# Kernel tuning notes

Hardware: AMD Instinct MI355X
Metric: run time of the kernel (lower is better)

Reference implementation:

```python
import jax, jax.numpy as jnp
import numpy as np

D_MODEL = 1024
N_REG = 8
D_REG = 32
LN_EPS = 1e-5


def setup_inputs() -> dict:
    key = jax.random.key(0)
    ks = jax.random.split(key, 14)
    s = 0.02
    return {
        "x": jax.random.normal(ks[0], (8, 2048, D_MODEL), dtype=jnp.float32),
        "ln_w": jnp.ones((D_MODEL,), jnp.float32),
        "ln_b": jnp.zeros((D_MODEL,), jnp.float32),
        "Wrq": jax.random.normal(ks[1], (N_REG, D_MODEL), jnp.float32) * s,
        "brq": jax.random.normal(ks[2], (N_REG,), jnp.float32) * s,
        "Wrp": jax.random.normal(ks[3], (D_MODEL, D_REG), jnp.float32) * s,
        "brp": jax.random.normal(ks[4], (D_MODEL,), jnp.float32) * s,
        "Wwq": jax.random.normal(ks[5], (N_REG, D_MODEL), jnp.float32) * s,
        "bwq": jax.random.normal(ks[6], (N_REG,), jnp.float32) * s,
        "Wwv": jax.random.normal(ks[7], (D_REG, D_MODEL), jnp.float32) * s,
        "bwv": jax.random.normal(ks[8], (D_REG,), jnp.float32) * s,
        "Wwg": jax.random.normal(ks[9], (1, D_MODEL), jnp.float32) * s,
        "bwg": jnp.full((1,), -3.0, jnp.float32),
        "mix": jnp.asarray(0.001, jnp.float32),
    }


def _layernorm(x, w, b):
    mu = jnp.mean(x, axis=-1, keepdims=True)
    var = jnp.mean(jnp.square(x - mu), axis=-1, keepdims=True)
    return (x - mu) * jax.lax.rsqrt(var + LN_EPS) * w + b


def _forward(x, ln_w, ln_b, Wrq, brq, Wrp, brp, Wwq, bwq, Wwv, bwv, Wwg, bwg, mix):
    B, L, D = x.shape
    h = _layernorm(x, ln_w, ln_b)  # (B,L,D)
    # Precompute all per-timestep projections as big GEMMs (same math as per-step Linear)
    r_w = jax.nn.softmax(jnp.einsum("bld,rd->blr", h, Wrq) + brq, axis=-1)  # (B,L,R)
    w_w = jax.nn.softmax(jnp.einsum("bld,rd->blr", h, Wwq) + bwq, axis=-1)  # (B,L,R)
    w_v = jnp.einsum("bld,kd->blk", h, Wwv) + bwv                           # (B,L,Dr)
    w_g = jax.nn.sigmoid(jnp.einsum("bld,od->blo", h, Wwg) + bwg)           # (B,L,1)

    def step(registers, inputs):
        rw_t, ww_t, wv_t, wg_t = inputs  # (B,R), (B,R), (B,Dr), (B,1)
        r_v = jnp.einsum("br,brd->bd", rw_t, registers)  # read (B,Dr)
        us = (ww_t * wg_t)[..., None]                     # (B,R,1)
        new_regs = (1.0 - us) * registers + us * wv_t[:, None, :]
        return new_regs, r_v

    init_regs = jnp.zeros((B, N_REG, D_REG), x.dtype)
    seq = (
        jnp.moveaxis(r_w, 1, 0),
        jnp.moveaxis(w_w, 1, 0),
        jnp.moveaxis(w_v, 1, 0),
        jnp.moveaxis(w_g, 1, 0),
    )
    _, r_vs = jax.lax.scan(step, init_regs, seq)  # (L,B,Dr)
    r_vs = jnp.moveaxis(r_vs, 0, 1)               # (B,L,Dr)
    r_out = jnp.einsum("blk,dk->bld", r_vs, Wrp) + brp  # read_proj
    return mix * r_out


def reference(x, ln_w, ln_b, Wrq, brq, Wrp, brp, Wwq, bwq, Wwv, bwv, Wwg, bwg, mix):
    return _forward(x, ln_w, ln_b, Wrq, brq, Wrp, brp, Wwq, bwq, Wwv, bwv, Wwg, bwg, mix)
```

## Files before the change

kernel.cpp:

```cpp
#include <hip/hip_runtime.h>

#define D_MODEL 1024
#define L_SEQ   2048
#define N_BATCH 8
#define N_TOK   (N_BATCH * L_SEQ)
#define N_REGS  8
#define D_REG   32
#define N_CHUNK 64
#define CHUNK   32
#define LN_EPS  1e-5f

__device__ __forceinline__ float wred(float v) {
    #pragma unroll
    for (int off = 32; off > 0; off >>= 1) v += __shfl_xor(v, off, 64);
    return v;
}

__device__ __forceinline__ float sigmoidf(float z) {
    return 1.f / (1.f + expf(-z));
}

__global__ __launch_bounds__(256) void k_prep(
    const float* __restrict__ ln_w, const float* __restrict__ ln_b,
    const float* __restrict__ Wrq,  const float* __restrict__ brq,
    const float* __restrict__ Wwq,  const float* __restrict__ bwq,
    const float* __restrict__ Wwv,  const float* __restrict__ bwv,
    const float* __restrict__ Wwg,  const float* __restrict__ bwg,
    float* __restrict__ Wpp, float* __restrict__ c1, float* __restrict__ c2)
{
    const int f = blockIdx.x;
    const int g = f / 13, i = f % 13;

    const float* wrow = nullptr; float bias = 0.f;
    if (f < 8)        { wrow = Wrq + f * D_MODEL;        bias = brq[f]; }
    else if (f < 16)  { wrow = Wwq + (f - 8) * D_MODEL;  bias = bwq[f - 8]; }
    else if (f == 16) { wrow = Wwg;                      bias = bwg[0]; }
    else if (f < 49)  { wrow = Wwv + (f - 17) * D_MODEL; bias = bwv[f - 17]; }

    float p1 = 0.f, p2 = 0.f;
    #pragma unroll
    for (int j = 0; j < 4; ++j) {
        const int k = j * 256 + threadIdx.x;
        float w  = wrow ? wrow[k] : 0.f;
        float wg = w * ln_w[k];
        Wpp[((size_t)(g * D_MODEL + k)) * 16 + i] = wg;
        p1 += wg;
        p2 = fmaf(w, ln_b[k], p2);
    }
    p1 = wred(p1); p2 = wred(p2);

    __shared__ float r1[4], r2[4];
    const int l = threadIdx.x & 63, w = threadIdx.x >> 6;
    if (l == 0) { r1[w] = p1; r2[w] = p2; }
    __syncthreads();
    if (threadIdx.x == 0) {
        c1[f] = r1[0] + r1[1] + r1[2] + r1[3];
        c2[f] = r2[0] + r2[1] + r2[2] + r2[3] + bias;
    }
}

__global__ __launch_bounds__(1024) void k_lnproj2(
    const float* __restrict__ x,
    const float* __restrict__ Wpp,
    const float* __restrict__ c1, const float* __restrict__ c2,
    float* __restrict__ rw_o, float* __restrict__ us_o, float* __restrict__ wv_o)
{
    const int tid  = threadIdx.x;
    const int lane = tid & 63;
    const int wv   = tid >> 6;
    const int g    = wv & 3;
    const int kh   = wv >> 2;
    const int tok  = blockIdx.x * 64 + lane;

    const int gs  = __builtin_amdgcn_readfirstlane(g);
    const int khs = __builtin_amdgcn_readfirstlane(kh);

    const float4* xr = reinterpret_cast<const float4*>(x + (size_t)tok * D_MODEL + khs * 256);
    const float4* wr = reinterpret_cast<const float4*>(Wpp) + (size_t)(gs * D_MODEL + khs * 256) * 4;

    float acc[13];
    #pragma unroll
    for (int i = 0; i < 13; ++i) acc[i] = 0.f;
    float sum = 0.f, ss = 0.f;

    for (int kk = 0; kk < 256; kk += 16) {
        float xb[16];
        #pragma unroll
        for (int u2 = 0; u2 < 4; ++u2) {
            float4 v = xr[(kk >> 2) + u2];
            xb[u2 * 4 + 0] = v.x; xb[u2 * 4 + 1] = v.y;
            xb[u2 * 4 + 2] = v.z; xb[u2 * 4 + 3] = v.w;
        }
        #pragma unroll
        for (int u = 0; u < 16; ++u) {
            const int k = kk + u;
            float4 wa = wr[k * 4 + 0];
            float4 wb = wr[k * 4 + 1];
            float4 wc = wr[k * 4 + 2];
            float  wd = reinterpret_cast<const float*>(wr + k * 4 + 3)[0];
            const float xs = xb[u];
            acc[0]  = fmaf(xs, wa.x, acc[0]);
            acc[1]  = fmaf(xs, wa.y, acc[1]);
            acc[2]  = fmaf(xs, wa.z, acc[2]);
            acc[3]  = fmaf(xs, wa.w, acc[3]);
            acc[4]  = fmaf(xs, wb.x, acc[4]);
            acc[5]  = fmaf(xs, wb.y, acc[5]);
            acc[6]  = fmaf(xs, wb.z, acc[6]);
            acc[7]  = fmaf(xs, wb.w, acc[7]);
            acc[8]  = fmaf(xs, wc.x, acc[8]);
            acc[9]  = fmaf(xs, wc.y, acc[9]);
            acc[10] = fmaf(xs, wc.z, acc[10]);
            acc[11] = fmaf(xs, wc.w, acc[11]);
            acc[12] = fmaf(xs, wd,   acc[12]);
            sum += xs;
            ss = fmaf(xs, xs, ss);
        }
    }

    __shared__ float S[64][56];
    if (kh == 0) {
        #pragma unroll
        for (int i = 0; i < 13; ++i) S[lane][g * 13 + i] = acc[i];
        if (g == 0) { S[lane][52] = sum; S[lane][53] = ss; }
    }
    __syncthreads();
    #pragma unroll
    for (int ph = 1; ph < 4; ++ph) {
        if (kh == ph) {
            #pragma unroll
            for (int i = 0; i < 13; ++i) S[lane][g * 13 + i] += acc[i];
            if (g == 0) { S[lane][52] += sum; S[lane][53] += ss; }
        }
        __syncthreads();
    }

    if (tid < 256) {
        const int t  = tid & 63;
        const int q  = tid >> 6;
        const int tg = blockIdx.x * 64 + t;

        const float tsum = S[t][52], tss = S[t][53];
        const float mu  = tsum * (1.f / D_MODEL);
        const float var = tss * (1.f / D_MODEL) - mu * mu;
        const float rs  = rsqrtf(var + LN_EPS);

        if (q == 0) {
            float lg[8];
            #pragma unroll
            for (int r = 0; r < 8; ++r)
                lg[r] = rs * (S[t][r] - mu * c1[r]) + c2[r];
            float m = lg[0];
            #pragma unroll
            for (int r = 1; r < 8; ++r) m = fmaxf(m, lg[r]);
            float sm = 0.f;
            #pragma unroll
            for (int r = 0; r < 8; ++r) { lg[r] = expf(lg[r] - m); sm += lg[r]; }
            float inv = 1.f / sm;
            float4* o = reinterpret_cast<float4*>(rw_o + (size_t)tg * 8);
            o[0] = make_float4(lg[0]*inv, lg[1]*inv, lg[2]*inv, lg[3]*inv);
            o[1] = make_float4(lg[4]*inv, lg[5]*inv, lg[6]*inv, lg[7]*inv);
        } else if (q == 1) {
            float lg[8];
            #pragma unroll
            for (int r = 0; r < 8; ++r)
                lg[r] = rs * (S[t][8 + r] - mu * c1[8 + r]) + c2[8 + r];
            float gl = rs * (S[t][16] - mu * c1[16]) + c2[16];
            float m = lg[0];
            #pragma unroll
            for (int r = 1; r < 8; ++r) m = fmaxf(m, lg[r]);
            float sm = 0.f;
            #pragma unroll
            for (int r = 0; r < 8; ++r) { lg[r] = expf(lg[r] - m); sm += lg[r]; }
            float inv = sigmoidf(gl) / sm;
            float4* o = reinterpret_cast<float4*>(us_o + (size_t)tg * 8);
            o[0] = make_float4(lg[0]*inv, lg[1]*inv, lg[2]*inv, lg[3]*inv);
            o[1] = make_float4(lg[4]*inv, lg[5]*inv, lg[6]*inv, lg[7]*inv);
        } else {
            const int f0 = 17 + (q - 2) * 16;
            float4* o = reinterpret_cast<float4*>(wv_o + (size_t)tg * 32 + (q - 2) * 16);
            #pragma unroll
            for (int jq = 0; jq < 4; ++jq) {
                float v0 = rs * (S[t][f0 + jq*4 + 0] - mu * c1[f0 + jq*4 + 0]) + c2[f0 + jq*4 + 0];
                float v1 = rs * (S[t][f0 + jq*4 + 1] - mu * c1[f0 + jq*4 + 1]) + c2[f0 + jq*4 + 1];
                float v2 = rs * (S[t][f0 + jq*4 + 2] - mu * c1[f0 + jq*4 + 2]) + c2[f0 + jq*4 + 2];
                float v3 = rs * (S[t][f0 + jq*4 + 3] - mu * c1[f0 + jq*4 + 3]) + c2[f0 + jq*4 + 3];
                o[jq] = make_float4(v0, v1, v2, v3);
            }
        }
    }
}

__global__ __launch_bounds__(256) void k_chunk(
    const float* __restrict__ us, const float* __restrict__ wv,
    float* __restrict__ A, float* __restrict__ Bc)
{
    const int gid  = blockIdx.x * 256 + threadIdx.x;
    const int k    = gid & 31;
    const int unit = gid >> 5;
    const int ch   = unit & 63;
    const int br   = unit >> 6;
    const int b    = br >> 3, r = br & 7;
    const int t0   = ch * CHUNK;

    const float* usp = us + ((size_t)(b * L_SEQ + t0)) * 8 + r;
    const float* wvp = wv + ((size_t)(b * L_SEQ + t0)) * 32 + k;

    float Aacc = 1.f, Bacc = 0.f;
    #pragma unroll 4
    for (int t = 0; t < CHUNK; ++t) {
        float u = usp[t * 8];
        float w = wvp[t * 32];
        float a = 1.f - u;
        Aacc *= a;
        Bacc = a * Bacc + u * w;
    }
    Bc[(size_t)unit * 32 + k] = Bacc;
    if (k == 0) A[unit] = Aacc;
}

__global__ __launch_bounds__(64) void k_chain(
    const float* __restrict__ A, const float* __restrict__ Bc,
    float* __restrict__ S0)
{
    const int gid = blockIdx.x * 64 + threadIdx.x;
    const int k   = gid & 31;
    const int br  = gid >> 5;
    float st = 0.f;
    #pragma unroll 4
    for (int ch = 0; ch < N_CHUNK; ++ch) {
        const int unit = br * N_CHUNK + ch;
        S0[(size_t)unit * 32 + k] = st;
        st = A[unit] * st + Bc[(size_t)unit * 32 + k];
    }
}

__global__ __launch_bounds__(64) void k_replay(
    const float* __restrict__ rw, const float* __restrict__ us,
    const float* __restrict__ wv, const float* __restrict__ S0,
    float* __restrict__ rvs)
{
    const int gid  = blockIdx.x * 64 + threadIdx.x;
    const int k    = gid & 31;
    const int unit = gid >> 5;
    const int ch   = unit & 63;
    const int b    = unit >> 6;

    float s[8];
    #pragma unroll
    for (int r = 0; r < 8; ++r)
        s[r] = S0[((size_t)((b * 8 + r) * N_CHUNK) + ch) * 32 + k];

    const int t0 = b * L_SEQ + ch * CHUNK;
    const float* rwp = rw + (size_t)t0 * 8;
    const float* usp = us + (size_t)t0 * 8;
    const float* wvp = wv + (size_t)t0 * 32 + k;
    float*       rvp = rvs + (size_t)t0 * 32 + k;

    for (int t = 0; t < CHUNK; ++t) {
        float4 rw0 = reinterpret_cast<const float4*>(rwp + t * 8)[0];
        float4 rw1 = reinterpret_cast<const float4*>(rwp + t * 8)[1];
        float4 us0 = reinterpret_cast<const float4*>(usp + t * 8)[0];
        float4 us1 = reinterpret_cast<const float4*>(usp + t * 8)[1];
        float  w   = wvp[t * 32];

        float rv = rw0.x*s[0] + rw0.y*s[1] + rw0.z*s[2] + rw0.w*s[3]
                 + rw1.x*s[4] + rw1.y*s[5] + rw1.z*s[6] + rw1.w*s[7];
        rvp[t * 32] = rv;

        s[0] = (1.f - us0.x)*s[0] + us0.x*w;
        s[1] = (1.f - us0.y)*s[1] + us0.y*w;
        s[2] = (1.f - us0.z)*s[2] + us0.z*w;
        s[3] = (1.f - us0.w)*s[3] + us0.w*w;
        s[4] = (1.f - us1.x)*s[4] + us1.x*w;
        s[5] = (1.f - us1.y)*s[5] + us1.y*w;
        s[6] = (1.f - us1.z)*s[6] + us1.z*w;
        s[7] = (1.f - us1.w)*s[7] + us1.w*w;
    }
}

__global__ __launch_bounds__(256) void k_outproj(
    const float* __restrict__ rvs, const float* __restrict__ Wrp,
    const float* __restrict__ brp, const float* __restrict__ mix_p,
    float* __restrict__ out)
{
    const int d    = blockIdx.y * 256 + threadIdx.x;
    const int tok0 = blockIdx.x * 64;

    float4 wr[8];
    #pragma unroll
    for (int q = 0; q < 8; ++q)
        wr[q] = reinterpret_cast<const float4*>(Wrp)[(size_t)d * 8 + q];

    const float bias = brp[d];
    const float mix  = mix_p[0];

    for (int t = 0; t < 64; ++t) {
        const float4* rv = reinterpret_cast<const float4*>(rvs + (size_t)(tok0 + t) * 32);
        float acc = 0.f;
        #pragma unroll
        for (int q = 0; q < 8; ++q) {
            float4 v = rv[q];
            acc += wr[q].x*v.x + wr[q].y*v.y + wr[q].z*v.z + wr[q].w*v.w;
        }
        out[(size_t)(tok0 + t) * D_MODEL + d] = mix * (acc + bias);
    }
}

extern "C" void kernel_launch(void* const* d_in, const int* in_sizes, int n_in,
                              void* d_out, int out_size, void* d_ws, size_t ws_size,
                              hipStream_t stream)
{
    const float* x    = (const float*)d_in[0];
    const float* ln_w = (const float*)d_in[1];
    const float* ln_b = (const float*)d_in[2];
    const float* Wrq  = (const float*)d_in[3];
    const float* brq  = (const float*)d_in[4];
    const float* Wrp  = (const float*)d_in[5];
    const float* brp  = (const float*)d_in[6];
    const float* Wwq  = (const float*)d_in[7];
    const float* bwq  = (const float*)d_in[8];
    const float* Wwv  = (const float*)d_in[9];
    const float* bwv  = (const float*)d_in[10];
    const float* Wwg  = (const float*)d_in[11];
    const float* bwg  = (const float*)d_in[12];
    const float* mix  = (const float*)d_in[13];
    float* out = (float*)d_out;

    float* ws   = (float*)d_ws;
    float* rw_b = ws;
    float* us_b = ws + 131072;
    float* wv_b = ws + 262144;
    float* A_b  = ws + 786432;
    float* B_b  = ws + 790528;
    float* S0_b = ws + 921600;
    float* rv_b = ws + 1052672;
    float* Wpp  = rv_b;
    float* c1_b = rv_b + 65536;
    float* c2_b = rv_b + 65600;

    k_prep<<<52, 256, 0, stream>>>(ln_w, ln_b, Wrq, brq, Wwq, bwq,
                                   Wwv, bwv, Wwg, bwg, Wpp, c1_b, c2_b);
    k_lnproj2<<<256, 1024, 0, stream>>>(x, Wpp, c1_b, c2_b, rw_b, us_b, wv_b);
    k_chunk <<<512, 256, 0, stream>>>(us_b, wv_b, A_b, B_b);
    k_chain <<<32,  64,  0, stream>>>(A_b, B_b, S0_b);
    k_replay<<<256, 64,  0, stream>>>(rw_b, us_b, wv_b, S0_b, rv_b);
    dim3 gc(N_TOK / 64, 4);
    k_outproj<<<gc, 256, 0, stream>>>(rv_b, Wrp, brp, mix, out);
}
```

Baseline: 97.52 us.

## Stage x tiles through double-buffered LDS with coalesced loads in LN-projection kernel

```diff
diff --git a/kernel.cpp b/kernel.cpp
--- a/kernel.cpp
+++ b/kernel.cpp
@@ -10,6 +10,11 @@
 #define CHUNK   32
 #define LN_EPS  1e-5f
 
+#define KC      32
+#define XSTR    65
+#define XQ      (KC * XSTR)
+#define SSTR    57
+
 __device__ __forceinline__ float wred(float v) {
     #pragma unroll
     for (int off = 32; off > 0; off >>= 1) v += __shfl_xor(v, off, 64);
@@ -59,77 +64,125 @@
     }
 }
 
-__global__ __launch_bounds__(1024) void k_lnproj2(
+template<int STATS>
+__device__ __forceinline__ void proj_chunk(
+    const float* __restrict__ lx,
+    const float4* __restrict__ wr0,
+    int lane, float acc[13], float& st)
+{
+    #pragma unroll 4
+    for (int k = 0; k < KC; ++k) {
+        const float xs = lx[k * XSTR + lane];
+        const float4* wr = wr0 + (k << 2);
+        float4 wa = wr[0], wb = wr[1], wc = wr[2];
+        float  wd = reinterpret_cast<const float*>(wr)[12];
+        acc[0]  = fmaf(xs, wa.x, acc[0]);
+        acc[1]  = fmaf(xs, wa.y, acc[1]);
+        acc[2]  = fmaf(xs, wa.z, acc[2]);
+        acc[3]  = fmaf(xs, wa.w, acc[3]);
+        acc[4]  = fmaf(xs, wb.x, acc[4]);
+        acc[5]  = fmaf(xs, wb.y, acc[5]);
+        acc[6]  = fmaf(xs, wb.z, acc[6]);
+        acc[7]  = fmaf(xs, wb.w, acc[7]);
+        acc[8]  = fmaf(xs, wc.x, acc[8]);
+        acc[9]  = fmaf(xs, wc.y, acc[9]);
+        acc[10] = fmaf(xs, wc.z, acc[10]);
+        acc[11] = fmaf(xs, wc.w, acc[11]);
+        acc[12] = fmaf(xs, wd,   acc[12]);
+        if (STATS == 1) st += xs;
+        if (STATS == 2) st = fmaf(xs, xs, st);
+    }
+}
+
+__global__ __launch_bounds__(1024) void k_lnproj3(
     const float* __restrict__ x,
     const float* __restrict__ Wpp,
     const float* __restrict__ c1, const float* __restrict__ c2,
     float* __restrict__ rw_o, float* __restrict__ us_o, float* __restrict__ wv_o)
 {
+    extern __shared__ float lds[];
+    float* Sb = lds + 2 * 4 * XQ;
+
     const int tid  = threadIdx.x;
     const int lane = tid & 63;
     const int wv   = tid >> 6;
     const int g    = wv & 3;
     const int kh   = wv >> 2;
-    const int tok  = blockIdx.x * 64 + lane;
+    const int tok0 = blockIdx.x * 64;
 
     const int gs  = __builtin_amdgcn_readfirstlane(g);
     const int khs = __builtin_amdgcn_readfirstlane(kh);
 
-    const float4* xr = reinterpret_cast<const float4*>(x + (size_t)tok * D_MODEL + khs * 256);
-    const float4* wr = reinterpret_cast<const float4*>(Wpp) + (size_t)(gs * D_MODEL + khs * 256) * 4;
-
+    const int tq  = tid & 255;
+    const int row = tq >> 3;
+    const int c4  = tq & 7;
+
+    const float4* x4 = reinterpret_cast<const float4*>(x);
+
+    float4 xg[2];
     float acc[13];
     #pragma unroll
     for (int i = 0; i < 13; ++i) acc[i] = 0.f;
-    float sum = 0.f, ss = 0.f;
-
-    for (int kk = 0; kk < 256; kk += 16) {
-        float xb[16];
+    float st = 0.f;
+
+    const size_t gbase = (size_t)(tok0 + row) * 256 + khs * 64 + c4;
+
+    {
+        xg[0] = x4[gbase];
+        xg[1] = x4[gbase + 32 * 256];
+        float* dst = lds + khs * XQ + (c4 * 4) * XSTR;
         #pragma unroll
-        for (int u2 = 0; u2 < 4; ++u2) {
-            float4 v = xr[(kk >> 2) + u2];
-            xb[u2 * 4 + 0] = v.x; xb[u2 * 4 + 1] = v.y;
-            xb[u2 * 4 + 2] = v.z; xb[u2 * 4 + 3] = v.w;
-        }
-        #pragma unroll
-        for (int u = 0; u < 16; ++u) {
-            const int k = kk + u;
-            float4 wa = wr[k * 4 + 0];
-            float4 wb = wr[k * 4 + 1];
-            float4 wc = wr[k * 4 + 2];
-            float  wd = reinterpret_cast<const float*>(wr + k * 4 + 3)[0];
-            const float xs = xb[u];
-            acc[0]  = fmaf(xs, wa.x, acc[0]);
-            acc[1]  = fmaf(xs, wa.y, acc[1]);
-            acc[2]  = fmaf(xs, wa.z, acc[2]);
-            acc[3]  = fmaf(xs, wa.w, acc[3]);
-            acc[4]  = fmaf(xs, wb.x, acc[4]);
-            acc[5]  = fmaf(xs, wb.y, acc[5]);
-            acc[6]  = fmaf(xs, wb.z, acc[6]);
-            acc[7]  = fmaf(xs, wb.w, acc[7]);
-            acc[8]  = fmaf(xs, wc.x, acc[8]);
-            acc[9]  = fmaf(xs, wc.y, acc[9]);
-            acc[10] = fmaf(xs, wc.z, acc[10]);
-            acc[11] = fmaf(xs, wc.w, acc[11]);
-            acc[12] = fmaf(xs, wd,   acc[12]);
-            sum += xs;
-            ss = fmaf(xs, xs, ss);
-        }
-    }
-
-    __shared__ float S[64][56];
+        for (int p = 0; p < 2; ++p) {
+            const int r = row + 32 * p;
+            dst[0 * XSTR + r] = xg[p].x;
+            dst[1 * XSTR + r] = xg[p].y;
+            dst[2 * XSTR + r] = xg[p].z;
+            dst[3 * XSTR + r] = xg[p].w;
+        }
+    }
+    __syncthreads();
+
+    for (int c = 0; c < 8; ++c) {
+        if (c < 7)  {
+            xg[0] = x4[gbase + (size_t)(c + 1) * 8];
+            xg[1] = x4[gbase + (size_t)(c + 1) * 8 + 32 * 256];
+        }
+
+        const float*  lx  = lds + ((c & 1) * 4 + khs) * XQ;
+        const float4* wr0 = reinterpret_cast<const float4*>(Wpp)
+                          + ((gs * D_MODEL + khs * 256 + c * KC) << 2);
+        if (gs == 1)      proj_chunk<1>(lx, wr0, lane, acc, st);
+        else if (gs == 2) proj_chunk<2>(lx, wr0, lane, acc, st);
+        else              proj_chunk<0>(lx, wr0, lane, acc, st);
+
+        if (c < 7) {
+            float* dst = lds + (((c + 1) & 1) * 4 + khs) * XQ + (c4 * 4) * XSTR;
+            #pragma unroll
+            for (int p = 0; p < 2; ++p) {
+                const int r = row + 32 * p;
+                dst[0 * XSTR + r] = xg[p].x;
+                dst[1 * XSTR + r] = xg[p].y;
+                dst[2 * XSTR + r] = xg[p].z;
+                dst[3 * XSTR + r] = xg[p].w;
+            }
+        }
+        __syncthreads();
+    }
+
     if (kh == 0) {
         #pragma unroll
-        for (int i = 0; i < 13; ++i) S[lane][g * 13 + i] = acc[i];
-        if (g == 0) { S[lane][52] = sum; S[lane][53] = ss; }
+        for (int i = 0; i < 13; ++i) Sb[lane * SSTR + g * 13 + i] = acc[i];
+        if (g == 1) Sb[lane * SSTR + 52] = st;
+        if (g == 2) Sb[lane * SSTR + 53] = st;
     }
     __syncthreads();
     #pragma unroll
     for (int ph = 1; ph < 4; ++ph) {
         if (kh == ph) {
             #pragma unroll
-            for (int i = 0; i < 13; ++i) S[lane][g * 13 + i] += acc[i];
-            if (g == 0) { S[lane][52] += sum; S[lane][53] += ss; }
+            for (int i = 0; i < 13; ++i) Sb[lane * SSTR + g * 13 + i] += acc[i];
+            if (g == 1) Sb[lane * SSTR + 52] += st;
+            if (g == 2) Sb[lane * SSTR + 53] += st;
         }
         __syncthreads();
     }
@@ -138,8 +191,9 @@
         const int t  = tid & 63;
         const int q  = tid >> 6;
         const int tg = blockIdx.x * 64 + t;
-
-        const float tsum = S[t][52], tss = S[t][53];
+        const float* St = Sb + t * SSTR;
+
+        const float tsum = St[52], tss = St[53];
         const float mu  = tsum * (1.f / D_MODEL);
         const float var = tss * (1.f / D_MODEL) - mu * mu;
         const float rs  = rsqrtf(var + LN_EPS);
@@ -148,7 +202,7 @@
             float lg[8];
             #pragma unroll
             for (int r = 0; r < 8; ++r)
-                lg[r] = rs * (S[t][r] - mu * c1[r]) + c2[r];
+                lg[r] = rs * (St[r] - mu * c1[r]) + c2[r];
             float m = lg[0];
             #pragma unroll
             for (int r = 1; r < 8; ++r) m = fmaxf(m, lg[r]);
@@ -163,8 +217,8 @@
             float lg[8];
             #pragma unroll
             for (int r = 0; r < 8; ++r)
-                lg[r] = rs * (S[t][8 + r] - mu * c1[8 + r]) + c2[8 + r];
-            float gl = rs * (S[t][16] - mu * c1[16]) + c2[16];
+                lg[r] = rs * (St[8 + r] - mu * c1[8 + r]) + c2[8 + r];
+            float gl = rs * (St[16] - mu * c1[16]) + c2[16];
             float m = lg[0];
             #pragma unroll
             for (int r = 1; r < 8; ++r) m = fmaxf(m, lg[r]);
@@ -180,10 +234,10 @@
             float4* o = reinterpret_cast<float4*>(wv_o + (size_t)tg * 32 + (q - 2) * 16);
             #pragma unroll
             for (int jq = 0; jq < 4; ++jq) {
-                float v0 = rs * (S[t][f0 + jq*4 + 0] - mu * c1[f0 + jq*4 + 0]) + c2[f0 + jq*4 + 0];
-                float v1 = rs * (S[t][f0 + jq*4 + 1] - mu * c1[f0 + jq*4 + 1]) + c2[f0 + jq*4 + 1];
-                float v2 = rs * (S[t][f0 + jq*4 + 2] - mu * c1[f0 + jq*4 + 2]) + c2[f0 + jq*4 + 2];
-                float v3 = rs * (S[t][f0 + jq*4 + 3] - mu * c1[f0 + jq*4 + 3]) + c2[f0 + jq*4 + 3];
+                float v0 = rs * (St[f0 + jq*4 + 0] - mu * c1[f0 + jq*4 + 0]) + c2[f0 + jq*4 + 0];
+                float v1 = rs * (St[f0 + jq*4 + 1] - mu * c1[f0 + jq*4 + 1]) + c2[f0 + jq*4 + 1];
+                float v2 = rs * (St[f0 + jq*4 + 2] - mu * c1[f0 + jq*4 + 2]) + c2[f0 + jq*4 + 2];
+                float v3 = rs * (St[f0 + jq*4 + 3] - mu * c1[f0 + jq*4 + 3]) + c2[f0 + jq*4 + 3];
                 o[jq] = make_float4(v0, v1, v2, v3);
             }
         }
@@ -338,9 +392,12 @@
     float* c1_b = rv_b + 65536;
     float* c2_b = rv_b + 65600;
 
+    const size_t lds_bytes = (size_t)(2 * 4 * XQ + 64 * SSTR) * 4;
+
     k_prep<<<52, 256, 0, stream>>>(ln_w, ln_b, Wrq, brq, Wwq, bwq,
                                    Wwv, bwv, Wwg, bwg, Wpp, c1_b, c2_b);
-    k_lnproj2<<<256, 1024, 0, stream>>>(x, Wpp, c1_b, c2_b, rw_b, us_b, wv_b);
+    k_lnproj3<<<256, 1024, lds_bytes, stream>>>(x, Wpp, c1_b, c2_b,
+                                                rw_b, us_b, wv_b);
     k_chunk <<<512, 256, 0, stream>>>(us_b, wv_b, A_b, B_b);
     k_chain <<<32,  64,  0, stream>>>(A_b, B_b, S0_b);
     k_replay<<<256, 64,  0, stream>>>(rw_b, us_b, wv_b, S0_b, rv_b);
```

Measured after the change: 94.99 us, median of 5. 1.03x faster.
